# Kernel tuning notes

Measured on AMD Instinct MI355X. Metric: run time of the kernel, lower is better.

## Reference

```python
import jax, jax.numpy as jnp
import numpy as np

HEAD_DIM = 32
KERNEL = 3
DILATION = 2
PAD = DILATION * (KERNEL - 1) // 2  # = 2
SCALE = HEAD_DIM ** (-0.5)


def _unfold(x):
    """Emulate nn.Unfold(kernel_size=KERNEL, dilation=DILATION, padding=PAD, stride=1).
    x: [B, C, H, W] -> [B, C, K*K, H, W] (channel-major, kernel positions inner,
    matching torch's C*K*K channel layout after the module's reshape)."""
    B, C, H, W = x.shape
    xp = jnp.pad(x, ((0, 0), (0, 0), (PAD, PAD), (PAD, PAD)))
    patches = [xp[:, :, i * DILATION:i * DILATION + H, j * DILATION:j * DILATION + W]
               for i in range(KERNEL) for j in range(KERNEL)]
    return jnp.stack(patches, axis=2)  # [B, C, K2, H, W]


def setup_inputs() -> dict:
    key = jax.random.key(0)
    kq, kk, kv = jax.random.split(key, 3)
    B, d, H, W = 4, 384, 64, 64
    q = jax.random.normal(kq, (B, d, H, W), dtype=jnp.float32)
    k = jax.random.normal(kk, (B, d, H, W), dtype=jnp.float32)
    v = jax.random.normal(kv, (B, d, H, W), dtype=jnp.float32)
    return {"q": q, "k": k, "v": v}


def reference(q, k, v):
    B, d, H, W = q.shape
    nh = d // HEAD_DIM
    K2 = KERNEL * KERNEL
    L = H * W
    # q: [B, nh, hd, L]
    qh = q.reshape(B, nh, HEAD_DIM, L)
    # unfolded k, v: [B, nh, hd, K2, L]
    ku = _unfold(k).reshape(B, nh, HEAD_DIM, K2, L)
    vu = _unfold(v).reshape(B, nh, HEAD_DIM, K2, L)
    # per-pixel attention logits: [B, nh, L, K2]
    attn = jnp.einsum('bncl,bnckl->bnlk', qh, ku) * SCALE
    attn = jax.nn.softmax(attn, axis=-1)
    # weighted values: [B, nh, L, hd]
    out = jnp.einsum('bnlk,bnckl->bnlc', attn, vu)
    # -> [B, L, nh, hd] -> [B, H, W, d]
    return out.transpose(0, 2, 1, 3).reshape(B, H, W, d)
```

## Files before the change

### kernel.cpp

```cpp
#include <hip/hip_runtime.h>
#include <hip/hip_bf16.h>


#define HD   32
#define NHD  12
#define DDIM 384
#define HH   64
#define WW   64
#define HWSZ 4096
#define SCALEF 0.17677669529663687f

__global__ __launch_bounds__(256) void dilate_attn(const float* __restrict__ q,
                                                   const float* __restrict__ k,
                                                   const float* __restrict__ v,
                                                   float* __restrict__ out) {
    const int tid = threadIdx.x;
    const int r   = tid >> 6;
    const int x   = tid & 63;
    const int bz  = blockIdx.x;
    const int bh  = bz >> 4;
    const int b   = bh / NHD;
    const int n   = bh - b * NHD;
    const int y   = (bz & 15) * 4 + r;

    const size_t chan_base = (size_t)(b * DDIM + n * HD) * HWSZ;
    const int pix = y * WW + x;

    int  toff[9];
    bool tval[9];
#pragma unroll
    for (int di = 0; di < 3; ++di) {
        int yy = y + 2 * di - 2;
        bool vy = (yy >= 0) && (yy < HH);
#pragma unroll
        for (int p = 0; p < 3; ++p) {
            int xo = x + 2 * p - 2;
            bool vx = (xo >= 0) && (xo < WW);
            bool ok = vy && vx;
            tval[di * 3 + p] = ok;
            toff[di * 3 + p] = ok ? (yy * WW + xo) : pix;
        }
    }

    const float* qb = q + chan_base + pix;
    float qreg[HD];
#pragma unroll
    for (int c = 0; c < HD; ++c) qreg[c] = qb[(size_t)c * HWSZ] * SCALEF;

    const float* kbase = k + chan_base;
    float l[9];
#pragma unroll
    for (int t = 0; t < 9; ++t) {
        const float* kt = kbase + toff[t];
        float a0 = 0.f, a1 = 0.f;
#pragma unroll
        for (int c = 0; c < HD; c += 2) {
            a0 += qreg[c]     * kt[(size_t)c * HWSZ];
            a1 += qreg[c + 1] * kt[(size_t)(c + 1) * HWSZ];
        }
        float acc = a0 + a1;
        l[t] = tval[t] ? acc : 0.f;
    }

    float m = l[0];
#pragma unroll
    for (int t = 1; t < 9; ++t) m = fmaxf(m, l[t]);
    float w[9], s = 0.f;
#pragma unroll
    for (int t = 0; t < 9; ++t) { w[t] = __expf(l[t] - m); s += w[t]; }
    float inv = 1.0f / s;
#pragma unroll
    for (int t = 0; t < 9; ++t) w[t] = tval[t] ? (w[t] * inv) : 0.f;

    const float* vbase = v + chan_base;
    float* ob = out + ((size_t)(b * HH + y) * WW + x) * DDIM + n * HD;

#pragma unroll
    for (int half = 0; half < 2; ++half) {
        const float* vh = vbase + (size_t)(half * 16) * HWSZ;
        float o[16];
#pragma unroll
        for (int c = 0; c < 16; ++c) o[c] = 0.f;
#pragma unroll
        for (int t = 0; t < 9; ++t) {
            const float* vt = vh + toff[t];
            float wt = w[t];
#pragma unroll
            for (int c = 0; c < 16; ++c) o[c] += wt * vt[(size_t)c * HWSZ];
        }
        float* oh = ob + half * 16;
        *(float4*)(oh)      = make_float4(o[0],  o[1],  o[2],  o[3]);
        *(float4*)(oh + 4)  = make_float4(o[4],  o[5],  o[6],  o[7]);
        *(float4*)(oh + 8)  = make_float4(o[8],  o[9],  o[10], o[11]);
        *(float4*)(oh + 12) = make_float4(o[12], o[13], o[14], o[15]);
    }
}

extern "C" void kernel_launch(void* const* d_in, const int* in_sizes, int n_in,
                              void* d_out, int out_size, void* d_ws, size_t ws_size,
                              hipStream_t stream) {
    const float* q = (const float*)d_in[0];
    const float* k = (const float*)d_in[1];
    const float* v = (const float*)d_in[2];
    float* out = (float*)d_out;
    hipLaunchKernelGGL(dilate_attn, dim3(768), dim3(256), 0, stream, q, k, v, out);
}
```

Before: 132.5 us.

## Split head channels across four thread groups with shared-memory logit reduction

Each block now handles a single image row, and its four 64-thread groups each take 8 of the 32 head channels. Each group writes partial q·k dot products for the 9 taps to shared memory. After a barrier every thread sums the partials, runs the softmax, and accumulates and stores its own 8 output channels. This quadruples the grid and cuts per-thread registers and serial load chains to raise occupancy and memory-level parallelism, with launch bounds hinting 6 blocks per CU. The cost is redundant softmax work across groups, a __syncthreads, and narrower 32-byte output stores per thread.

```diff
diff --git a/kernel.cpp b/kernel.cpp
--- a/kernel.cpp
+++ b/kernel.cpp
@@ -10,18 +10,18 @@
 #define HWSZ 4096
 #define SCALEF 0.17677669529663687f
 
-__global__ __launch_bounds__(256) void dilate_attn(const float* __restrict__ q,
-                                                   const float* __restrict__ k,
-                                                   const float* __restrict__ v,
-                                                   float* __restrict__ out) {
+__global__ __launch_bounds__(256, 6) void dilate_attn(const float* __restrict__ q,
+                                                      const float* __restrict__ k,
+                                                      const float* __restrict__ v,
+                                                      float* __restrict__ out) {
     const int tid = threadIdx.x;
-    const int r   = tid >> 6;
     const int x   = tid & 63;
+    const int g   = tid >> 6;
     const int bz  = blockIdx.x;
-    const int bh  = bz >> 4;
+    const int bh  = bz >> 6;
     const int b   = bh / NHD;
     const int n   = bh - b * NHD;
-    const int y   = (bz & 15) * 4 + r;
+    const int y   = bz & 63;
 
     const size_t chan_base = (size_t)(b * DDIM + n * HD) * HWSZ;
     const int pix = y * WW + x;
@@ -35,33 +35,40 @@
 #pragma unroll
         for (int p = 0; p < 3; ++p) {
             int xo = x + 2 * p - 2;
-            bool vx = (xo >= 0) && (xo < WW);
-            bool ok = vy && vx;
+            bool ok = vy && (xo >= 0) && (xo < WW);
             tval[di * 3 + p] = ok;
             toff[di * 3 + p] = ok ? (yy * WW + xo) : pix;
         }
     }
 
-    const float* qb = q + chan_base + pix;
-    float qreg[HD];
+    const size_t goff = (size_t)(g * 8) * HWSZ;
+    const float* qb = q + chan_base + goff + pix;
+    float qreg[8];
 #pragma unroll
-    for (int c = 0; c < HD; ++c) qreg[c] = qb[(size_t)c * HWSZ] * SCALEF;
+    for (int c = 0; c < 8; ++c) qreg[c] = qb[(size_t)c * HWSZ];
 
-    const float* kbase = k + chan_base;
+    __shared__ float part[36 * 64];
+    const float* kb = k + chan_base + goff;
+#pragma unroll
+    for (int t = 0; t < 9; ++t) {
+        const float* kt = kb + toff[t];
+        float a0 = 0.f, a1 = 0.f;
+#pragma unroll
+        for (int c = 0; c < 8; c += 2) {
+            a0 += qreg[c]     * kt[(size_t)c * HWSZ];
+            a1 += qreg[c + 1] * kt[(size_t)(c + 1) * HWSZ];
+        }
+        part[(t * 4 + g) * 64 + x] = a0 + a1;
+    }
+    __syncthreads();
+
     float l[9];
 #pragma unroll
     for (int t = 0; t < 9; ++t) {
-        const float* kt = kbase + toff[t];
-        float a0 = 0.f, a1 = 0.f;
-#pragma unroll
-        for (int c = 0; c < HD; c += 2) {
-            a0 += qreg[c]     * kt[(size_t)c * HWSZ];
-            a1 += qreg[c + 1] * kt[(size_t)(c + 1) * HWSZ];
-        }
-        float acc = a0 + a1;
-        l[t] = tval[t] ? acc : 0.f;
+        float s = part[(t * 4 + 0) * 64 + x] + part[(t * 4 + 1) * 64 + x]
+                + part[(t * 4 + 2) * 64 + x] + part[(t * 4 + 3) * 64 + x];
+        l[t] = tval[t] ? (s * SCALEF) : 0.f;
     }
-
     float m = l[0];
 #pragma unroll
     for (int t = 1; t < 9; ++t) m = fmaxf(m, l[t]);
@@ -72,28 +79,21 @@
 #pragma unroll
     for (int t = 0; t < 9; ++t) w[t] = tval[t] ? (w[t] * inv) : 0.f;
 
-    const float* vbase = v + chan_base;
-    float* ob = out + ((size_t)(b * HH + y) * WW + x) * DDIM + n * HD;
+    const float* vb = v + chan_base + goff;
+    float o[8];
+#pragma unroll
+    for (int c = 0; c < 8; ++c) o[c] = 0.f;
+#pragma unroll
+    for (int t = 0; t < 9; ++t) {
+        const float* vt = vb + toff[t];
+        float wt = w[t];
+#pragma unroll
+        for (int c = 0; c < 8; ++c) o[c] += wt * vt[(size_t)c * HWSZ];
+    }
 
-#pragma unroll
-    for (int half = 0; half < 2; ++half) {
-        const float* vh = vbase + (size_t)(half * 16) * HWSZ;
-        float o[16];
-#pragma unroll
-        for (int c = 0; c < 16; ++c) o[c] = 0.f;
-#pragma unroll
-        for (int t = 0; t < 9; ++t) {
-            const float* vt = vh + toff[t];
-            float wt = w[t];
-#pragma unroll
-            for (int c = 0; c < 16; ++c) o[c] += wt * vt[(size_t)c * HWSZ];
-        }
-        float* oh = ob + half * 16;
-        *(float4*)(oh)      = make_float4(o[0],  o[1],  o[2],  o[3]);
-        *(float4*)(oh + 4)  = make_float4(o[4],  o[5],  o[6],  o[7]);
-        *(float4*)(oh + 8)  = make_float4(o[8],  o[9],  o[10], o[11]);
-        *(float4*)(oh + 12) = make_float4(o[12], o[13], o[14], o[15]);
-    }
+    float* ob = out + ((size_t)(b * HWSZ) + pix) * DDIM + n * HD + g * 8;
+    *(float4*)(ob)     = make_float4(o[0], o[1], o[2], o[3]);
+    *(float4*)(ob + 4) = make_float4(o[4], o[5], o[6], o[7]);
 }
 
 extern "C" void kernel_launch(void* const* d_in, const int* in_sizes, int n_in,
@@ -103,5 +103,5 @@
     const float* k = (const float*)d_in[1];
     const float* v = (const float*)d_in[2];
     float* out = (float*)d_out;
-    hipLaunchKernelGGL(dilate_attn, dim3(768), dim3(256), 0, stream, q, k, v, out);
+    hipLaunchKernelGGL(dilate_attn, dim3(3072), dim3(256), 0, stream, q, k, v, out);
 }
```

Result: slower. 179.6 us (+35.6%).
